# Performance work log

Measured on AMD Instinct MI355X. Metric: run time of the kernel, lower is better.

## Reference

```python
import jax, jax.numpy as jnp
import numpy as np

N_EMBD = 1024
N_HEAD = 16


def setup_inputs() -> dict:
    key = jax.random.key(0)
    k1, k2, k3 = jax.random.split(key, 3)
    x = jax.random.normal(k1, (4, 2048, N_EMBD), dtype=jnp.float32)
    w_attn = jax.random.normal(k2, (N_EMBD, 3 * N_EMBD), dtype=jnp.float32) * (N_EMBD ** -0.5)
    w_proj = jax.random.normal(k3, (N_EMBD, N_EMBD), dtype=jnp.float32) * (N_EMBD ** -0.5)
    return {"x": x, "w_attn": w_attn, "w_proj": w_proj}


def reference(x, w_attn, w_proj):
    B, T, C = x.shape
    H = N_HEAD
    D = C // H  # head dim
    qkv = x @ w_attn  # [B,T,3C]
    q, k, v = jnp.split(qkv, 3, axis=-1)
    # [B,T,C] -> [B,H,T,D]
    q = q.reshape(B, T, H, D).transpose(0, 2, 1, 3)
    k = k.reshape(B, T, H, D).transpose(0, 2, 1, 3)
    v = v.reshape(B, T, H, D).transpose(0, 2, 1, 3)
    scale = 1.0 / jnp.sqrt(jnp.asarray(D, dtype=x.dtype))
    att = jnp.einsum('bhqd,bhkd->bhqk', q, k) * scale  # [B,H,T,T]
    causal = jnp.tril(jnp.ones((T, T), dtype=bool))
    att = jnp.where(causal, att, jnp.asarray(-jnp.inf, dtype=att.dtype))
    att = jax.nn.softmax(att, axis=-1)
    y = jnp.einsum('bhqk,bhkd->bhqd', att, v)  # [B,H,T,D]
    y = y.transpose(0, 2, 1, 3).reshape(B, T, C)
    return y @ w_proj
```

## Files before the change

### kernel.cpp

```cpp
#include <hip/hip_runtime.h>
#include <math.h>


typedef unsigned short ushort_t;
typedef __attribute__((ext_vector_type(8))) short bf16x8;
typedef __attribute__((ext_vector_type(4))) float f32x4;

#define MFMA16(a, b, c) __builtin_amdgcn_mfma_f32_16x16x32_bf16((a), (b), (c), 0, 0, 0)

#define CP_ASYNC16(lds, gp)                                                        \
    __builtin_amdgcn_global_load_lds(                                              \
        (const __attribute__((address_space(1))) void*)(gp),                       \
        (__attribute__((address_space(3))) void*)(lds), 16, 0, 0)

#define SCALE2 0.1803368801111204f

#define BAR() __builtin_amdgcn_s_barrier()
#define WAITBAR2()                                           \
    do {                                                     \
        asm volatile("s_waitcnt vmcnt(2)" ::: "memory");     \
        __builtin_amdgcn_s_barrier();                        \
    } while (0)
#define WAITBAR0()                                           \
    do {                                                     \
        asm volatile("s_waitcnt vmcnt(0)" ::: "memory");     \
        __builtin_amdgcn_s_barrier();                        \
    } while (0)

__device__ __forceinline__ ushort_t bf16r(float x) {
    unsigned int u = __float_as_uint(x);
    u += 0x7FFFu + ((u >> 16) & 1u);
    return (ushort_t)(u >> 16);
}

__device__ __forceinline__ unsigned cvt_pk_bf16(float lo, float hi) {
    unsigned r;
    asm("v_cvt_pk_bf16_f32 %0, %1, %2" : "=v"(r) : "v"(lo), "v"(hi));
    return r;
}
__device__ __forceinline__ void pl32_swap(unsigned& a, unsigned& c) {
    asm("v_permlane32_swap_b32 %0, %1" : "+v"(a), "+v"(c));
}
__device__ __forceinline__ void pl16_swap(unsigned& a, unsigned& c) {
    asm("v_permlane16_swap_b32 %0, %1" : "+v"(a), "+v"(c));
}


__global__ __launch_bounds__(256) void cast_f32_bf16(const float4* __restrict__ src,
                                                     ushort4* __restrict__ dst) {
    int i = blockIdx.x * 256 + threadIdx.x;
    float4 v = src[i];
    ushort4 o;
    o.x = bf16r(v.x); o.y = bf16r(v.y); o.z = bf16r(v.z); o.w = bf16r(v.w);
    dst[i] = o;
}

__global__ __launch_bounds__(256) void transpose_cast(const float* __restrict__ src,
                                                      ushort_t* __restrict__ dst,
                                                      int R, int Cc) {
    __shared__ float tile[32][33];
    const int tx = threadIdx.x, ty = threadIdx.y;
    const int c0 = blockIdx.x * 32, r0 = blockIdx.y * 32;
#pragma unroll
    for (int i = 0; i < 4; ++i)
        tile[ty + i * 8][tx] = src[(size_t)(r0 + ty + i * 8) * Cc + c0 + tx];
    __syncthreads();
#pragma unroll
    for (int i = 0; i < 4; ++i)
        dst[(size_t)(c0 + ty + i * 8) * R + r0 + tx] = bf16r(tile[tx][ty + i * 8]);
}

__global__ __launch_bounds__(512, 2)
void gemm_8ph(const ushort_t* __restrict__ A, const ushort_t* __restrict__ Bt,
              int K, int mode,
              ushort_t* __restrict__ Qh, ushort_t* __restrict__ Kh,
              ushort_t* __restrict__ Vt, float* __restrict__ Cout, int nbx) {
    __shared__ __align__(16) ushort_t As[2][16384];
    __shared__ __align__(16) ushort_t Bs[2][8192];
    const int tid = threadIdx.x;
    const int l = tid & 63, w = tid >> 6;
    const int lm = l & 15, lq = l >> 4;
    const int wm = w >> 1, wn = w & 1;

    int bid = blockIdx.x;
    const int cpx = gridDim.x >> 3;
    bid = (bid & 7) * cpx + (bid >> 3);
    const int by = bid / nbx, bx = bid - by * nbx;
    const int row0 = by * 256, col0 = bx * 128;

    const int srow = tid >> 3, sslot = tid & 7;
    const int ssw = (sslot ^ (srow & 7)) * 8;
    const ushort_t* gA = A + (size_t)(row0 + srow) * K + ssw;
    const ushort_t* gB = Bt + (size_t)(col0 + srow) * K + ssw;

    auto stageA = [&](int dbuf, int hm, int T) {
        const ushort_t* s = gA + (size_t)(hm * 128) * K + T * 64;
        CP_ASYNC16(&As[dbuf][hm * 8192 + tid * 8], s);
        CP_ASYNC16(&As[dbuf][hm * 8192 + 4096 + tid * 8], s + (size_t)64 * K);
    };
    auto stageB = [&](int dbuf, int T) {
        const ushort_t* s = gB + T * 64;
        CP_ASYNC16(&Bs[dbuf][tid * 8], s);
        CP_ASYNC16(&Bs[dbuf][4096 + tid * 8], s + (size_t)64 * K);
    };

    const int arow0 = wm * 64 + lm;
    const int brow0 = wn * 64 + lm;
    const int lsw = lm & 7;

    f32x4 acc[4][4];
#pragma unroll
    for (int i = 0; i < 4; ++i)
#pragma unroll
        for (int j = 0; j < 4; ++j) acc[i][j] = (f32x4){0.f, 0.f, 0.f, 0.f};

    bf16x8 af[2][2];
    bf16x8 bq[2][2][2];

    auto ldA = [&](int d, int qm) {
#pragma unroll
        for (int mf = 0; mf < 2; ++mf) {
            const int r = arow0 + qm * 32 + mf * 16;
#pragma unroll
            for (int ks = 0; ks < 2; ++ks)
                af[mf][ks] =
                    *(const bf16x8*)(&As[d][r * 64 + (((ks << 2) | lq) ^ lsw) * 8]);
        }
    };
    auto ldB = [&](int d) {
#pragma unroll
        for (int qn = 0; qn < 2; ++qn)
#pragma unroll
            for (int nf = 0; nf < 2; ++nf) {
                const int r = brow0 + qn * 32 + nf * 16;
#pragma unroll
                for (int ks = 0; ks < 2; ++ks)
                    bq[qn][nf][ks] =
                        *(const bf16x8*)(&Bs[d][r * 64 + (((ks << 2) | lq) ^ lsw) * 8]);
            }
    };
    auto mma = [&](int qm) {
        __builtin_amdgcn_s_setprio(1);
#pragma unroll
        for (int mf = 0; mf < 2; ++mf)
#pragma unroll
            for (int qn = 0; qn < 2; ++qn)
#pragma unroll
                for (int nf = 0; nf < 2; ++nf) {
                    f32x4 c = acc[qm * 2 + mf][qn * 2 + nf];
                    c = MFMA16(af[mf][0], bq[qn][nf][0], c);
                    c = MFMA16(af[mf][1], bq[qn][nf][1], c);
                    acc[qm * 2 + mf][qn * 2 + nf] = c;
                }
        __builtin_amdgcn_s_setprio(0);
    };

    stageA(0, 0, 0); stageA(0, 1, 0);
    stageB(0, 0);
    stageB(1, 1);

    const int ntiles = K >> 6;
    const int niter = ntiles >> 1;

    for (int it = 0; it < niter; ++it) {
        const int tE = 2 * it, tO = tE + 1;
        const bool s2 = (tE + 2) < ntiles;
        const bool s3 = (tE + 3) < ntiles;

        WAITBAR2();
        ldA(0, 0); ldB(0);
        stageA(1, 0, tO);
        BAR();
        mma(0);
        BAR();
        ldA(0, 1);
        stageA(1, 1, tO);
        if (s2) stageB(0, tE + 2);
        BAR();
        mma(1);
        BAR();

        if (it + 1 < niter) { WAITBAR2(); } else { WAITBAR0(); }
        ldA(1, 0); ldB(1);
        if (s2) stageA(0, 0, tE + 2);
        BAR();
        mma(0);
        BAR();
        ldA(1, 1);
        if (s2) stageA(0, 1, tE + 2);
        if (s3) stageB(1, tE + 3);
        BAR();
        mma(1);
        BAR();
    }

    if (mode == 1) {
#pragma unroll
        for (int im = 0; im < 4; ++im)
#pragma unroll
            for (int jn = 0; jn < 4; ++jn)
#pragma unroll
                for (int reg = 0; reg < 4; ++reg) {
                    const int rr = row0 + wm * 64 + im * 16 + lq * 4 + reg;
                    const int cc = col0 + wn * 64 + jn * 16 + lm;
                    Cout[(size_t)rr * 1024 + cc] = acc[im][jn][reg];
                }
    } else {
#pragma unroll
        for (int im = 0; im < 4; ++im) {
#pragma unroll
            for (int jn = 0; jn < 4; ++jn) {
#pragma unroll
                for (int reg = 0; reg < 4; ++reg) {
                    const int rr = row0 + wm * 64 + im * 16 + lq * 4 + reg;
                    const int cc = col0 + wn * 64 + jn * 16 + lm;
                    const float v = acc[im][jn][reg];
                    const int b = rr >> 11, t = rr & 2047;
                    if (cc < 1024) {
                        const int h = cc >> 6, d = cc & 63;
                        Qh[((size_t)(b * 16 + h) * 2048 + t) * 64 + d] =
                            bf16r(v * SCALE2);
                    } else if (cc < 2048) {
                        const int c2 = cc - 1024, h = c2 >> 6, d = c2 & 63;
                        Kh[((size_t)(b * 16 + h) * 2048 + t) * 64 + d] = bf16r(v);
                    } else {
                        const int c2 = cc - 2048, h = c2 >> 6, d = c2 & 63;
                        Vt[((size_t)(b * 16 + h) * 64 + d) * 2048 + t] = bf16r(v);
                    }
                }
            }
        }
    }
}

__global__ __launch_bounds__(256, 4)
void attn_mfma(const ushort_t* __restrict__ Qh, const ushort_t* __restrict__ Kh,
               const ushort_t* __restrict__ Vt, ushort_t* __restrict__ Y) {
    __shared__ ushort_t Ks[2][4096];
    __shared__ ushort_t Vs[2][4096];
    const int tid = threadIdx.x, l = tid & 63, w = tid >> 6;
    const int lm = l & 15, lq = l >> 4;
    const int bh = blockIdx.x;
    const int pr = blockIdx.y;
    const int qbA = pr, qbB = 31 - pr;
    const int b = bh >> 4, h = bh & 15;
    const f32x4 zero4 = {0.f, 0.f, 0.f, 0.f};
    const short oneb = (short)0x3F80;
    const bf16x8 onesf = {oneb, oneb, oneb, oneb, oneb, oneb, oneb, oneb};
    const int lqs8 = (lq ^ ((lm >> 1) & 3)) * 8;

    bf16x8 qf[2][2];
    {
        const ushort_t* qA = Qh + ((size_t)bh * 2048 + qbA * 64 + w * 16 + lm) * 64 + lq * 8;
        const ushort_t* qB = Qh + ((size_t)bh * 2048 + qbB * 64 + w * 16 + lm) * 64 + lq * 8;
        qf[0][0] = *(const bf16x8*)(qA);
        qf[0][1] = *(const bf16x8*)(qA + 32);
        qf[1][0] = *(const bf16x8*)(qB);
        qf[1][1] = *(const bf16x8*)(qB + 32);
    }

    f32x4 O[2][4], Ol[2];
#pragma unroll
    for (int q = 0; q < 2; ++q) {
        Ol[q] = zero4;
#pragma unroll
        for (int i = 0; i < 4; ++i) O[q][i] = zero4;
    }

    const int srow = tid >> 2, slot = tid & 3;
    const int srcoff = ((slot ^ ((srow >> 1) & 3)) * 8);
    const ushort_t* gKr = Kh + ((size_t)bh * 2048 + srow) * 64 + srcoff;
    const ushort_t* gVr = Vt + ((size_t)bh * 64 + srow) * 2048 + srcoff;

    auto prefetch = [&](int jbn, int dbuf) {
        const ushort_t* gk = gKr + (size_t)jbn * 4096;
        const ushort_t* gv = gVr + jbn * 64;
        CP_ASYNC16(&Ks[dbuf][tid * 8], gk);
        CP_ASYNC16(&Ks[dbuf][2048 + tid * 8], gk + 32);
        CP_ASYNC16(&Vs[dbuf][tid * 8], gv);
        CP_ASYNC16(&Vs[dbuf][2048 + tid * 8], gv + 32);
    };

    auto sstep = [&](const bf16x8 (&kf)[4][2], const bf16x8 (&qfr)[2],
                     f32x4 (&st)[4]) {
#pragma unroll
        for (int n = 0; n < 4; ++n) {
            f32x4 s_acc = zero4;
            s_acc = MFMA16(kf[n][0], qfr[0], s_acc);
            s_acc = MFMA16(kf[n][1], qfr[1], s_acc);
            st[n] = s_acc;
        }
    };

    auto softmax = [&](const f32x4 (&st)[4], bool diag,
                       bf16x8& pf0, bf16x8& pf1) {
        float p[4][4];
#pragma unroll
        for (int n = 0; n < 4; ++n)
#pragma unroll
            for (int reg = 0; reg < 4; ++reg)
                p[n][reg] = __builtin_amdgcn_exp2f(st[n][reg]);
        if (diag) {
            const int qloc = w * 16 + lm;
#pragma unroll
            for (int n = 0; n < 4; ++n)
#pragma unroll
                for (int reg = 0; reg < 4; ++reg)
                    if (n * 16 + lq * 4 + reg > qloc) p[n][reg] = 0.f;
        }
        unsigned cpk[4][2];
#pragma unroll
        for (int n = 0; n < 4; ++n) {
            cpk[n][0] = cvt_pk_bf16(p[n][0], p[n][1]);
            cpk[n][1] = cvt_pk_bf16(p[n][2], p[n][3]);
        }
        union U8 { unsigned u[4]; bf16x8 v; };
        {
            unsigned z00 = cpk[0][0], z10 = cpk[1][0];
            unsigned z01 = cpk[0][1], z11 = cpk[1][1];
            pl32_swap(z00, z10); pl16_swap(z00, z10);
            pl32_swap(z01, z11); pl16_swap(z01, z11);
            U8 t0; t0.u[0] = z00; t0.u[1] = z01; t0.u[2] = z10; t0.u[3] = z11;
            pf0 = t0.v;
            unsigned y00 = cpk[2][0], y10 = cpk[3][0];
            unsigned y01 = cpk[2][1], y11 = cpk[3][1];
            pl32_swap(y00, y10); pl16_swap(y00, y10);
            pl32_swap(y01, y11); pl16_swap(y01, y11);
            U8 t1; t1.u[0] = y00; t1.u[1] = y01; t1.u[2] = y10; t1.u[3] = y11;
            pf1 = t1.v;
        }
    };

    auto pv = [&](const bf16x8& pf0, const bf16x8& pf1,
                  const bf16x8 (&vf)[4][2], f32x4 (&Or)[4], f32x4& Olr) {
#pragma unroll
        for (int dn = 0; dn < 4; ++dn) {
            Or[dn] = MFMA16(pf0, vf[dn][0], Or[dn]);
            Or[dn] = MFMA16(pf1, vf[dn][1], Or[dn]);
        }
        Olr = MFMA16(pf0, onesf, Olr);
        Olr = MFMA16(pf1, onesf, Olr);
    };

    prefetch(0, 0);
    for (int jb = 0; jb <= qbB; ++jb) {
        const int buf = jb & 1;
        __syncthreads();
        if (jb < qbB) prefetch(jb + 1, buf ^ 1);

        const ushort_t* Kb = Ks[buf];
        const ushort_t* Vb = Vs[buf];
        const bool dual = (jb <= qbA);

        bf16x8 kf[4][2];
#pragma unroll
        for (int n = 0; n < 4; ++n) {
            kf[n][0] = *(const bf16x8*)(Kb + (n * 16 + lm) * 32 + lqs8);
            kf[n][1] = *(const bf16x8*)(Kb + 2048 + (n * 16 + lm) * 32 + lqs8);
        }

        f32x4 stB[4], stA[4];
        __builtin_amdgcn_s_setprio(1);
        sstep(kf, qf[1], stB);
        if (dual) sstep(kf, qf[0], stA);
        __builtin_amdgcn_s_setprio(0);

        bf16x8 pfB0, pfB1;
        softmax(stB, jb == qbB, pfB0, pfB1);

        bf16x8 vf[4][2];
#pragma unroll
        for (int dn = 0; dn < 4; ++dn) {
            vf[dn][0] = *(const bf16x8*)(Vb + (dn * 16 + lm) * 32 + lqs8);
            vf[dn][1] = *(const bf16x8*)(Vb + 2048 + (dn * 16 + lm) * 32 + lqs8);
        }
#pragma unroll
        for (int dn = 0; dn < 4; ++dn) {
            asm volatile("" : "+v"(vf[dn][0]));
            asm volatile("" : "+v"(vf[dn][1]));
        }

        __builtin_amdgcn_s_setprio(1);
        pv(pfB0, pfB1, vf, O[1], Ol[1]);
        __builtin_amdgcn_s_setprio(0);

        if (dual) {
            bf16x8 pfA0, pfA1;
            softmax(stA, jb == qbA, pfA0, pfA1);
            __builtin_amdgcn_s_setprio(1);
            pv(pfA0, pfA1, vf, O[0], Ol[0]);
            __builtin_amdgcn_s_setprio(0);
        }
    }

#pragma unroll
    for (int qs = 0; qs < 2; ++qs) {
        const int tq = (qs ? qbB : qbA) * 64;
#pragma unroll
        for (int reg = 0; reg < 4; ++reg) {
            const float inv = 1.f / Ol[qs][reg];
            const size_t row = (size_t)b * 2048 + tq + w * 16 + lq * 4 + reg;
#pragma unroll
            for (int dn = 0; dn < 4; ++dn)
                Y[row * 1024 + h * 64 + dn * 16 + lm] = bf16r(O[qs][dn][reg] * inv);
        }
    }
}


extern "C" void kernel_launch(void* const* d_in, const int* in_sizes, int n_in,
                              void* d_out, int out_size, void* d_ws, size_t ws_size,
                              hipStream_t stream) {
    const float* x      = (const float*)d_in[0];
    const float* w_attn = (const float*)d_in[1];
    const float* w_proj = (const float*)d_in[2];
    float* out = (float*)d_out;

    char* ws = (char*)d_ws;
    ushort_t* xb   = (ushort_t*)(ws);
    ushort_t* watT = (ushort_t*)(ws + 16777216);
    ushort_t* wpjT = (ushort_t*)(ws + 23068672);
    ushort_t* Qh   = (ushort_t*)(ws + 25165824);
    ushort_t* Kh   = (ushort_t*)(ws + 41943040);
    ushort_t* Vt   = (ushort_t*)(ws + 58720256);
    ushort_t* Y    = (ushort_t*)(ws + 75497472);

    hipLaunchKernelGGL(cast_f32_bf16, dim3(8192), dim3(256), 0, stream,
                       (const float4*)x, (ushort4*)xb);
    hipLaunchKernelGGL(transpose_cast, dim3(96, 32), dim3(32, 8), 0, stream,
                       w_attn, watT, 1024, 3072);
    hipLaunchKernelGGL(transpose_cast, dim3(32, 32), dim3(32, 8), 0, stream,
                       w_proj, wpjT, 1024, 1024);

    hipLaunchKernelGGL(gemm_8ph, dim3(768), dim3(512), 0, stream,
                       xb, watT, 1024, 0, Qh, Kh, Vt, (float*)nullptr, 24);

    hipLaunchKernelGGL(attn_mfma, dim3(64, 16), dim3(256), 0, stream,
                       Qh, Kh, Vt, Y);

    hipLaunchKernelGGL(gemm_8ph, dim3(256), dim3(512), 0, stream,
                       Y, wpjT, 1024, 1, (ushort_t*)nullptr, (ushort_t*)nullptr,
                       (ushort_t*)nullptr, out, 8);
}
```

Measured before the change: 247.3 us.

## Triple-buffer global-to-LDS prefetch in GEMM and attention kernels

The GEMM main loop moves from a split A/B double buffer with half-tile staging to a three-stage ring buffer. Each stage loads a full A and B K-tile two tiles ahead, and vmcnt(6) lets one tile's loads stay in flight. The attention kernel likewise gets a three-slot K/V ring with a two-block-ahead prefetch and a vmcnt-based wait, replacing the per-iteration __syncthreads. This is meant to hide more global memory latency. In exchange it uses more LDS per block and lowers attention occupancy from 4 to 3 blocks per CU.

Result: slower. 277.1 us (+12.1%).

```diff
diff --git a/kernel.cpp b/kernel.cpp
--- a/kernel.cpp
+++ b/kernel.cpp
@@ -16,9 +16,9 @@
 #define SCALE2 0.1803368801111204f
 
 #define BAR() __builtin_amdgcn_s_barrier()
-#define WAITBAR2()                                           \
+#define WAITBAR6()                                           \
     do {                                                     \
-        asm volatile("s_waitcnt vmcnt(2)" ::: "memory");     \
+        asm volatile("s_waitcnt vmcnt(6)" ::: "memory");     \
         __builtin_amdgcn_s_barrier();                        \
     } while (0)
 #define WAITBAR0()                                           \
@@ -75,8 +75,8 @@
               int K, int mode,
               ushort_t* __restrict__ Qh, ushort_t* __restrict__ Kh,
               ushort_t* __restrict__ Vt, float* __restrict__ Cout, int nbx) {
-    __shared__ __align__(16) ushort_t As[2][16384];
-    __shared__ __align__(16) ushort_t Bs[2][8192];
+    __shared__ __align__(16) ushort_t As[3][16384];
+    __shared__ __align__(16) ushort_t Bs[3][8192];
     const int tid = threadIdx.x;
     const int l = tid & 63, w = tid >> 6;
     const int lm = l & 15, lq = l >> 4;
@@ -93,15 +93,15 @@
     const ushort_t* gA = A + (size_t)(row0 + srow) * K + ssw;
     const ushort_t* gB = Bt + (size_t)(col0 + srow) * K + ssw;
 
-    auto stageA = [&](int dbuf, int hm, int T) {
-        const ushort_t* s = gA + (size_t)(hm * 128) * K + T * 64;
-        CP_ASYNC16(&As[dbuf][hm * 8192 + tid * 8], s);
-        CP_ASYNC16(&As[dbuf][hm * 8192 + 4096 + tid * 8], s + (size_t)64 * K);
-    };
-    auto stageB = [&](int dbuf, int T) {
-        const ushort_t* s = gB + T * 64;
-        CP_ASYNC16(&Bs[dbuf][tid * 8], s);
-        CP_ASYNC16(&Bs[dbuf][4096 + tid * 8], s + (size_t)64 * K);
+    auto stage = [&](int dbuf, int T) {
+        const ushort_t* sA = gA + T * 64;
+        CP_ASYNC16(&As[dbuf][tid * 8], sA);
+        CP_ASYNC16(&As[dbuf][4096 + tid * 8], sA + (size_t)64 * K);
+        CP_ASYNC16(&As[dbuf][8192 + tid * 8], sA + (size_t)128 * K);
+        CP_ASYNC16(&As[dbuf][12288 + tid * 8], sA + (size_t)192 * K);
+        const ushort_t* sB = gB + T * 64;
+        CP_ASYNC16(&Bs[dbuf][tid * 8], sB);
+        CP_ASYNC16(&Bs[dbuf][4096 + tid * 8], sB + (size_t)64 * K);
     };
 
     const int arow0 = wm * 64 + lm;
@@ -155,43 +155,26 @@
         __builtin_amdgcn_s_setprio(0);
     };
 
-    stageA(0, 0, 0); stageA(0, 1, 0);
-    stageB(0, 0);
-    stageB(1, 1);
+    stage(0, 0);
+    stage(1, 1);
 
     const int ntiles = K >> 6;
-    const int niter = ntiles >> 1;
-
-    for (int it = 0; it < niter; ++it) {
-        const int tE = 2 * it, tO = tE + 1;
-        const bool s2 = (tE + 2) < ntiles;
-        const bool s3 = (tE + 3) < ntiles;
-
-        WAITBAR2();
-        ldA(0, 0); ldB(0);
-        stageA(1, 0, tO);
+    int cur = 0;
+    for (int t = 0; t < ntiles; ++t) {
+        if (t + 1 < ntiles) { WAITBAR6(); } else { WAITBAR0(); }
+        if (t + 2 < ntiles) {
+            int nb = cur + 2; if (nb >= 3) nb -= 3;
+            stage(nb, t + 2);
+        }
+        ldA(cur, 0); ldB(cur);
         BAR();
         mma(0);
         BAR();
-        ldA(0, 1);
-        stageA(1, 1, tO);
-        if (s2) stageB(0, tE + 2);
+        ldA(cur, 1);
         BAR();
         mma(1);
         BAR();
-
-        if (it + 1 < niter) { WAITBAR2(); } else { WAITBAR0(); }
-        ldA(1, 0); ldB(1);
-        if (s2) stageA(0, 0, tE + 2);
-        BAR();
-        mma(0);
-        BAR();
-        ldA(1, 1);
-        if (s2) stageA(0, 1, tE + 2);
-        if (s3) stageB(1, tE + 3);
-        BAR();
-        mma(1);
-        BAR();
+        ++cur; if (cur == 3) cur = 0;
     }
 
     if (mode == 1) {
@@ -233,11 +216,11 @@
     }
 }
 
-__global__ __launch_bounds__(256, 4)
+__global__ __launch_bounds__(256, 3)
 void attn_mfma(const ushort_t* __restrict__ Qh, const ushort_t* __restrict__ Kh,
                const ushort_t* __restrict__ Vt, ushort_t* __restrict__ Y) {
-    __shared__ ushort_t Ks[2][4096];
-    __shared__ ushort_t Vs[2][4096];
+    __shared__ ushort_t Ks[3][4096];
+    __shared__ ushort_t Vs[3][4096];
     const int tid = threadIdx.x, l = tid & 63, w = tid >> 6;
     const int lm = l & 15, lq = l >> 4;
     const int bh = blockIdx.x;
@@ -343,13 +326,23 @@
     };
 
     prefetch(0, 0);
+    prefetch(1, 1);
+
+    int cur = 0;
     for (int jb = 0; jb <= qbB; ++jb) {
-        const int buf = jb & 1;
-        __syncthreads();
-        if (jb < qbB) prefetch(jb + 1, buf ^ 1);
-
-        const ushort_t* Kb = Ks[buf];
-        const ushort_t* Vb = Vs[buf];
+        if (jb + 1 <= qbB) {
+            asm volatile("s_waitcnt vmcnt(4)" ::: "memory");
+        } else {
+            asm volatile("s_waitcnt vmcnt(0)" ::: "memory");
+        }
+        __builtin_amdgcn_s_barrier();
+        if (jb + 2 <= qbB) {
+            int nb = cur + 2; if (nb >= 3) nb -= 3;
+            prefetch(jb + 2, nb);
+        }
+
+        const ushort_t* Kb = Ks[cur];
+        const ushort_t* Vb = Vs[cur];
         const bool dual = (jb <= qbA);
 
         bf16x8 kf[4][2];
@@ -391,6 +384,8 @@
             pv(pfA0, pfA1, vf, O[0], Ol[0]);
             __builtin_amdgcn_s_setprio(0);
         }
+
+        ++cur; if (cur == 3) cur = 0;
     }
 
 #pragma unroll
```
